# Optimization experiments

Measured on AMD Instinct MI355X. Metric: run time of the kernel, lower is better.

## Reference

```python
import jax, jax.numpy as jnp
import numpy as np

B, C, H, W = 8, 10, 128, 128  # batch, hidden_dim, spatial
EPS = 1e-5


def conv1x1(x, w, b=None):
    # x: [b, i, h, w], w: [o, i] -> [b, o, h, w]
    y = jnp.einsum('oi,bihw->bohw', w, x)
    if b is not None:
        y = y + b[None, :, None, None]
    return y


def bn(x, gamma, beta):
    # training-mode batchnorm over (N, H, W), as InPlaceABNSync(activation='none')
    m = x.mean(axis=(0, 2, 3), keepdims=True)
    v = x.var(axis=(0, 2, 3), keepdims=True)
    xn = (x - m) * jax.lax.rsqrt(v + EPS)
    return xn * gamma[None, :, None, None] + beta[None, :, None, None]


def conv_gru(x, h, wg, bg, wc):
    # ConvGRU with 1x1 kernels: gates conv -> 2 channels (reset, update)
    gates = conv1x1(jnp.concatenate([x, h], axis=1), wg, bg)  # [b,2,h,w]
    reset = jax.nn.sigmoid(gates[:, 0:1])
    update = jax.nn.sigmoid(gates[:, 1:2])
    cand = jnp.tanh(conv1x1(jnp.concatenate([x, reset * h], axis=1), wc))
    return (1.0 - update) * h + update * cand


def setup_inputs() -> dict:
    key = jax.random.key(0)
    ks = jax.random.split(key, 16)
    rn = lambda k, shape, s=1.0: jax.random.normal(k, shape, dtype=jnp.float32) * s
    inp = {
        'f0': rn(ks[0], (B, C, H, W)),
        'f1': rn(ks[1], (B, C, H, W)),
        'h0': rn(ks[2], (B, C, H, W)),
        'h1': rn(ks[3], (B, C, H, W)),
        'h2': rn(ks[4], (B, C, H, W)),
        # Composition.comp_att: Conv2d(2C -> 1, bias=True) + Sigmoid
        'W_att': rn(ks[5], (1, 2 * C), 0.1),
        'b_att': jnp.zeros((1,), jnp.float32),
        # Composition.relation: Conv(2C->2C, no bias) BN ReLU Conv(2C->C, no bias) BN ReLU
        'W_r1': rn(ks[6], (2 * C, 2 * C), 0.1),
        'g_r1': jnp.ones((2 * C,), jnp.float32),
        'be_r1': jnp.zeros((2 * C,), jnp.float32),
        'W_r2': rn(ks[7], (C, 2 * C), 0.1),
        'g_r2': jnp.ones((C,), jnp.float32),
        'be_r2': jnp.zeros((C,), jnp.float32),
        # ConvGRU update[0]: gates Conv(2C->2, bias) ; candidate Conv(2C->C, no bias)
        'Wg0': rn(ks[8], (2, 2 * C), 0.1),
        'bg0': jnp.zeros((2,), jnp.float32),
        'Wc0': rn(ks[9], (C, 2 * C), 0.1),
        # ConvGRU update[1]
        'Wg1': rn(ks[10], (2, 2 * C), 0.1),
        'bg1': jnp.zeros((2,), jnp.float32),
        'Wc1': rn(ks[11], (C, 2 * C), 0.1),
    }
    return inp


def reference(f0, f1, h0, h1, h2,
              W_att, b_att, W_r1, g_r1, be_r1, W_r2, g_r2, be_r2,
              Wg0, bg0, Wc0, Wg1, bg1, Wc1):
    # node 0: update[0](h_node_list[0], f_node_list[0])
    node0 = conv_gru(h0, f0, Wg0, bg0, Wc0)
    # Composition over children h1, h2
    comp_att = jax.nn.sigmoid(conv1x1(jnp.concatenate([h1, h2], axis=1), W_att, b_att))  # [b,1,h,w]
    x = jnp.concatenate([f1, (h1 + h2) * comp_att], axis=1)  # [b,2C,h,w]
    x = jax.nn.relu(bn(conv1x1(x, W_r1), g_r1, be_r1))
    comp_full = jax.nn.relu(bn(conv1x1(x, W_r2), g_r2, be_r2))  # [b,C,h,w]
    # node 1: update[1](comp_full, f_node_list[1])
    node1 = conv_gru(comp_full, f1, Wg1, bg1, Wc1)
    return node0, node1, comp_att
```

## Files before the change

### kernel.cpp

```cpp
#include <hip/hip_runtime.h>
#include <math.h>

#define HW     16384
#define CDIM   10
#define NPIX   131072
#define NPLANE 1310720
#define BN_N   131072.0f
#define EPS_BN 1e-5f

__device__ __forceinline__ float sigf(float x) { return 1.0f / (1.0f + __expf(-x)); }
__device__ __forceinline__ float tanh_fast(float x) {
    x = fminf(fmaxf(x, -15.0f), 15.0f);
    float e = __expf(2.0f * x);
    return (e - 1.0f) / (e + 1.0f);
}

template<int CTRL>
__device__ __forceinline__ float dpp_add(float x) {
    int t = __builtin_amdgcn_update_dpp(0, __float_as_int(x), CTRL, 0xF, 0xF, true);
    return x + __int_as_float(t);
}
__device__ __forceinline__ float wred63(float x) {
    x = dpp_add<0x111>(x);
    x = dpp_add<0x112>(x);
    x = dpp_add<0x114>(x);
    x = dpp_add<0x118>(x);
    x = dpp_add<0x142>(x);
    x = dpp_add<0x143>(x);
    return x;
}

__global__ __launch_bounds__(256) void kernA(
    const float* __restrict__ f0, const float* __restrict__ f1,
    const float* __restrict__ h0, const float* __restrict__ h1, const float* __restrict__ h2,
    const float* __restrict__ W_att, const float* __restrict__ b_att,
    const float* __restrict__ W_r1,
    const float* __restrict__ Wg0, const float* __restrict__ bg0, const float* __restrict__ Wc0,
    float* __restrict__ node0, float* __restrict__ att_out, float* __restrict__ stats1)
{
    __shared__ float sPart[4 * 40];
    const int tid = threadIdx.x;
    const int p = blockIdx.x * 256 + tid;
    const int b = p >> 14, s = p & 16383;
    const int base = b * (CDIM * HW) + s;
    const int wave = tid >> 6, lane = tid & 63;

    float vh1[10], vh2[10], vf1[10], vf0[10], vh0[10];
#pragma unroll
    for (int c = 0; c < 10; c++) {
        vh1[c] = h1[base + c * HW];
        vh2[c] = h2[base + c * HW];
        vf1[c] = f1[base + c * HW];
        vf0[c] = f0[base + c * HW];
        vh0[c] = h0[base + c * HW];
    }

    float g0 = bg0[0], g1 = bg0[1];
#pragma unroll
    for (int i = 0; i < 10; i++) {
        g0 = fmaf(Wg0[i],      vh0[i], fmaf(Wg0[10 + i], vf0[i], g0));
        g1 = fmaf(Wg0[20 + i], vh0[i], fmaf(Wg0[30 + i], vf0[i], g1));
    }
    const float r = sigf(g0), u = sigf(g1);
#pragma unroll
    for (int o = 0; o < 10; o++) {
        float acc = 0.0f;
#pragma unroll
        for (int i = 0; i < 10; i++) acc = fmaf(Wc0[o * 20 + i], vh0[i], acc);
#pragma unroll
        for (int i = 0; i < 10; i++) acc = fmaf(Wc0[o * 20 + 10 + i], r * vf0[i], acc);
        node0[base + o * HW] = (1.0f - u) * vf0[o] + u * tanh_fast(acc);
    }

    float z = b_att[0];
#pragma unroll
    for (int c = 0; c < 10; c++) z = fmaf(W_att[c], vh1[c], fmaf(W_att[10 + c], vh2[c], z));
    const float att = sigf(z);
    att_out[p] = att;

    float x[20];
#pragma unroll
    for (int c = 0; c < 10; c++) { x[c] = vf1[c]; x[10 + c] = (vh1[c] + vh2[c]) * att; }
#pragma unroll
    for (int o = 0; o < 20; o++) {
        float acc = 0.0f;
#pragma unroll
        for (int i = 0; i < 20; i++) acc = fmaf(W_r1[o * 20 + i], x[i], acc);
        float rs = wred63(acc);
        float rq = wred63(acc * acc);
        if (lane == 63) { sPart[wave * 40 + o] = rs; sPart[wave * 40 + 20 + o] = rq; }
    }
    __syncthreads();
    if (tid < 40) {
        float t = sPart[tid] + sPart[40 + tid] + sPart[80 + tid] + sPart[120 + tid];
        atomicAdd(&stats1[tid], t);
    }
}

__global__ __launch_bounds__(256) void kernC(
    const float* __restrict__ f1, const float* __restrict__ h1, const float* __restrict__ h2,
    const float* __restrict__ W_att, const float* __restrict__ b_att,
    const float* __restrict__ W_r1, const float* __restrict__ g_r1, const float* __restrict__ be_r1,
    const float* __restrict__ W_r2,
    const float* __restrict__ stats1, float* __restrict__ y2out, float* __restrict__ stats2)
{
    __shared__ float sPart[4 * 20];
    const int tid = threadIdx.x;
    const int p = blockIdx.x * 256 + tid;
    const int b = p >> 14, s = p & 16383;
    const int base = b * (CDIM * HW) + s;
    const int wave = tid >> 6, lane = tid & 63;

    float A1[20], B1[20];
#pragma unroll
    for (int c = 0; c < 20; c++) {
        float mean = stats1[c] * (1.0f / BN_N);
        float var  = stats1[20 + c] * (1.0f / BN_N) - mean * mean;
        float a = g_r1[c] * rsqrtf(var + EPS_BN);
        A1[c] = a;
        B1[c] = be_r1[c] - mean * a;
    }

    float vh1[10], vh2[10], vf1[10];
#pragma unroll
    for (int c = 0; c < 10; c++) {
        vh1[c] = h1[base + c * HW];
        vh2[c] = h2[base + c * HW];
        vf1[c] = f1[base + c * HW];
    }
    float z = b_att[0];
#pragma unroll
    for (int c = 0; c < 10; c++) z = fmaf(W_att[c], vh1[c], fmaf(W_att[10 + c], vh2[c], z));
    const float att = sigf(z);

    float x[20];
#pragma unroll
    for (int c = 0; c < 10; c++) { x[c] = vf1[c]; x[10 + c] = (vh1[c] + vh2[c]) * att; }
    float x2[20];
#pragma unroll
    for (int o = 0; o < 20; o++) {
        float acc = 0.0f;
#pragma unroll
        for (int i = 0; i < 20; i++) acc = fmaf(W_r1[o * 20 + i], x[i], acc);
        x2[o] = fmaxf(fmaf(A1[o], acc, B1[o]), 0.0f);
    }
    const int base2 = b * (10 * HW) + s;
#pragma unroll
    for (int o = 0; o < 10; o++) {
        float acc = 0.0f;
#pragma unroll
        for (int i = 0; i < 20; i++) acc = fmaf(W_r2[o * 20 + i], x2[i], acc);
        y2out[base2 + o * HW] = acc;
        float rs = wred63(acc);
        float rq = wred63(acc * acc);
        if (lane == 63) { sPart[wave * 20 + o] = rs; sPart[wave * 20 + 10 + o] = rq; }
    }
    __syncthreads();
    if (tid < 20) {
        float t = sPart[tid] + sPart[20 + tid] + sPart[40 + tid] + sPart[60 + tid];
        atomicAdd(&stats2[tid], t);
    }
}

__global__ __launch_bounds__(256) void kernE(
    const float* __restrict__ f1, const float* __restrict__ y2in,
    const float* __restrict__ stats2,
    const float* __restrict__ g_r2, const float* __restrict__ be_r2,
    const float* __restrict__ Wg1, const float* __restrict__ bg1, const float* __restrict__ Wc1,
    float* __restrict__ node1)
{
    const int tid = threadIdx.x;
    const int p = blockIdx.x * 256 + tid;
    const int b = p >> 14, s = p & 16383;
    const int base = b * (CDIM * HW) + s;

    float A2[10], B2[10];
#pragma unroll
    for (int c = 0; c < 10; c++) {
        float mean = stats2[c] * (1.0f / BN_N);
        float var  = stats2[10 + c] * (1.0f / BN_N) - mean * mean;
        float a = g_r2[c] * rsqrtf(var + EPS_BN);
        A2[c] = a;
        B2[c] = be_r2[c] - mean * a;
    }

    float comp[10], vf1[10];
#pragma unroll
    for (int c = 0; c < 10; c++) {
        vf1[c]  = f1[base + c * HW];
        comp[c] = fmaxf(fmaf(A2[c], y2in[base + c * HW], B2[c]), 0.0f);
    }
    float g0 = bg1[0], g1v = bg1[1];
#pragma unroll
    for (int i = 0; i < 10; i++) {
        g0  = fmaf(Wg1[i],      comp[i], fmaf(Wg1[10 + i], vf1[i], g0));
        g1v = fmaf(Wg1[20 + i], comp[i], fmaf(Wg1[30 + i], vf1[i], g1v));
    }
    const float r = sigf(g0), u = sigf(g1v);
#pragma unroll
    for (int o = 0; o < 10; o++) {
        float acc = 0.0f;
#pragma unroll
        for (int i = 0; i < 10; i++) acc = fmaf(Wc1[o * 20 + i], comp[i], acc);
#pragma unroll
        for (int i = 0; i < 10; i++) acc = fmaf(Wc1[o * 20 + 10 + i], r * vf1[i], acc);
        node1[base + o * HW] = (1.0f - u) * vf1[o] + u * tanh_fast(acc);
    }
}

extern "C" void kernel_launch(void* const* d_in, const int* in_sizes, int n_in,
                              void* d_out, int out_size, void* d_ws, size_t ws_size,
                              hipStream_t stream) {
    const float* f0    = (const float*)d_in[0];
    const float* f1    = (const float*)d_in[1];
    const float* h0    = (const float*)d_in[2];
    const float* h1    = (const float*)d_in[3];
    const float* h2    = (const float*)d_in[4];
    const float* W_att = (const float*)d_in[5];
    const float* b_att = (const float*)d_in[6];
    const float* W_r1  = (const float*)d_in[7];
    const float* g_r1  = (const float*)d_in[8];
    const float* be_r1 = (const float*)d_in[9];
    const float* W_r2  = (const float*)d_in[10];
    const float* g_r2  = (const float*)d_in[11];
    const float* be_r2 = (const float*)d_in[12];
    const float* Wg0   = (const float*)d_in[13];
    const float* bg0   = (const float*)d_in[14];
    const float* Wc0   = (const float*)d_in[15];
    const float* Wg1   = (const float*)d_in[16];
    const float* bg1   = (const float*)d_in[17];
    const float* Wc1   = (const float*)d_in[18];

    float* out   = (float*)d_out;
    float* node0 = out;
    float* node1 = out + NPLANE;
    float* attO  = out + 2 * NPLANE;

    float* y2     = (float*)d_ws;
    float* stats1 = y2 + (size_t)10 * NPIX;
    float* stats2 = stats1 + 40;

    hipMemsetAsync(stats1, 0, 64 * sizeof(float), stream);

    dim3 grid(NPIX / 256), blk(256);
    kernA<<<grid, blk, 0, stream>>>(f0, f1, h0, h1, h2, W_att, b_att, W_r1,
                                    Wg0, bg0, Wc0, node0, attO, stats1);
    kernC<<<grid, blk, 0, stream>>>(f1, h1, h2, W_att, b_att, W_r1, g_r1, be_r1, W_r2,
                                    stats1, y2, stats2);
    kernE<<<grid, blk, 0, stream>>>(f1, y2, stats2, g_r2, be_r2, Wg1, bg1, Wc1,
                                    node1);
}
```

Measured before the change: 148.8 us.

## Fuse three kernels into one cooperative kernel with grid-wide syncs for BN stats

Replaces the three-kernel pipeline with a single cooperative kernel of 256 blocks by 512 threads, where each thread owns one pixel. Per-block partial BN sums are written to a workspace and reduced after grid.sync(), which removes the atomics and the memset. Each thread keeps its conv activations in registers, so the recompute of attention and conv1 in the second pass, the y2 round-trip through global memory, and the reloads of f1/h1/h2 all go away. The cost is two grid-wide barriers, high register pressure from holding many live values under launch bounds of 512 threads with 2 blocks per CU, and a hard requirement that all 256 blocks be co-resident.

```diff
diff --git a/kernel.cpp b/kernel.cpp
--- a/kernel.cpp
+++ b/kernel.cpp
@@ -1,5 +1,8 @@
 #include <hip/hip_runtime.h>
+#include <hip/hip_cooperative_groups.h>
 #include <math.h>
+
+namespace cg = cooperative_groups;
 
 #define HW     16384
 #define CDIM   10
@@ -7,6 +10,8 @@
 #define NPLANE 1310720
 #define BN_N   131072.0f
 #define EPS_BN 1e-5f
+#define NBLK   256
+#define NTHR   512
 
 __device__ __forceinline__ float sigf(float x) { return 1.0f / (1.0f + __expf(-x)); }
 __device__ __forceinline__ float tanh_fast(float x) {
@@ -30,17 +35,23 @@
     return x;
 }
 
-__global__ __launch_bounds__(256) void kernA(
+__global__ __launch_bounds__(NTHR, 2) void fused(
     const float* __restrict__ f0, const float* __restrict__ f1,
     const float* __restrict__ h0, const float* __restrict__ h1, const float* __restrict__ h2,
     const float* __restrict__ W_att, const float* __restrict__ b_att,
-    const float* __restrict__ W_r1,
+    const float* __restrict__ W_r1, const float* __restrict__ g_r1, const float* __restrict__ be_r1,
+    const float* __restrict__ W_r2, const float* __restrict__ g_r2, const float* __restrict__ be_r2,
     const float* __restrict__ Wg0, const float* __restrict__ bg0, const float* __restrict__ Wc0,
-    float* __restrict__ node0, float* __restrict__ att_out, float* __restrict__ stats1)
+    const float* __restrict__ Wg1, const float* __restrict__ bg1, const float* __restrict__ Wc1,
+    float* __restrict__ node0, float* __restrict__ node1, float* __restrict__ att_out,
+    float* __restrict__ part1, float* __restrict__ part2)
 {
-    __shared__ float sPart[4 * 40];
+    cg::grid_group grid = cg::this_grid();
+    __shared__ float sPart[8 * 40];
+    __shared__ float sRed[40];
     const int tid = threadIdx.x;
-    const int p = blockIdx.x * 256 + tid;
+    const int bid = blockIdx.x;
+    const int p = bid * NTHR + tid;
     const int b = p >> 14, s = p & 16383;
     const int base = b * (CDIM * HW) + s;
     const int wave = tid >> 6, lane = tid & 63;
@@ -55,21 +66,23 @@
         vh0[c] = h0[base + c * HW];
     }
 
-    float g0 = bg0[0], g1 = bg0[1];
-#pragma unroll
-    for (int i = 0; i < 10; i++) {
-        g0 = fmaf(Wg0[i],      vh0[i], fmaf(Wg0[10 + i], vf0[i], g0));
-        g1 = fmaf(Wg0[20 + i], vh0[i], fmaf(Wg0[30 + i], vf0[i], g1));
-    }
-    const float r = sigf(g0), u = sigf(g1);
-#pragma unroll
-    for (int o = 0; o < 10; o++) {
-        float acc = 0.0f;
-#pragma unroll
-        for (int i = 0; i < 10; i++) acc = fmaf(Wc0[o * 20 + i], vh0[i], acc);
-#pragma unroll
-        for (int i = 0; i < 10; i++) acc = fmaf(Wc0[o * 20 + 10 + i], r * vf0[i], acc);
-        node0[base + o * HW] = (1.0f - u) * vf0[o] + u * tanh_fast(acc);
+    {
+        float g0 = bg0[0], g1 = bg0[1];
+#pragma unroll
+        for (int i = 0; i < 10; i++) {
+            g0 = fmaf(Wg0[i],      vh0[i], fmaf(Wg0[10 + i], vf0[i], g0));
+            g1 = fmaf(Wg0[20 + i], vh0[i], fmaf(Wg0[30 + i], vf0[i], g1));
+        }
+        const float r = sigf(g0), u = sigf(g1);
+#pragma unroll
+        for (int o = 0; o < 10; o++) {
+            float acc = 0.0f;
+#pragma unroll
+            for (int i = 0; i < 10; i++) acc = fmaf(Wc0[o * 20 + i], vh0[i], acc);
+#pragma unroll
+            for (int i = 0; i < 10; i++) acc = fmaf(Wc0[o * 20 + 10 + i], r * vf0[i], acc);
+            node0[base + o * HW] = (1.0f - u) * vf0[o] + u * tanh_fast(acc);
+        }
     }
 
     float z = b_att[0];
@@ -81,114 +94,80 @@
     float x[20];
 #pragma unroll
     for (int c = 0; c < 10; c++) { x[c] = vf1[c]; x[10 + c] = (vh1[c] + vh2[c]) * att; }
+    float acc1[20];
 #pragma unroll
     for (int o = 0; o < 20; o++) {
         float acc = 0.0f;
 #pragma unroll
         for (int i = 0; i < 20; i++) acc = fmaf(W_r1[o * 20 + i], x[i], acc);
+        acc1[o] = acc;
         float rs = wred63(acc);
         float rq = wred63(acc * acc);
         if (lane == 63) { sPart[wave * 40 + o] = rs; sPart[wave * 40 + 20 + o] = rq; }
     }
     __syncthreads();
     if (tid < 40) {
-        float t = sPart[tid] + sPart[40 + tid] + sPart[80 + tid] + sPart[120 + tid];
-        atomicAdd(&stats1[tid], t);
-    }
-}
-
-__global__ __launch_bounds__(256) void kernC(
-    const float* __restrict__ f1, const float* __restrict__ h1, const float* __restrict__ h2,
-    const float* __restrict__ W_att, const float* __restrict__ b_att,
-    const float* __restrict__ W_r1, const float* __restrict__ g_r1, const float* __restrict__ be_r1,
-    const float* __restrict__ W_r2,
-    const float* __restrict__ stats1, float* __restrict__ y2out, float* __restrict__ stats2)
-{
-    __shared__ float sPart[4 * 20];
-    const int tid = threadIdx.x;
-    const int p = blockIdx.x * 256 + tid;
-    const int b = p >> 14, s = p & 16383;
-    const int base = b * (CDIM * HW) + s;
-    const int wave = tid >> 6, lane = tid & 63;
-
+        float t = 0.0f;
+#pragma unroll
+        for (int w = 0; w < 8; w++) t += sPart[w * 40 + tid];
+        part1[tid * NBLK + bid] = t;
+    }
+    grid.sync();
+
+    for (int ch = wave; ch < 40; ch += 8) {
+        float v = part1[ch * NBLK + lane]       + part1[ch * NBLK + lane + 64]
+                + part1[ch * NBLK + lane + 128] + part1[ch * NBLK + lane + 192];
+        v = wred63(v);
+        if (lane == 63) sRed[ch] = v;
+    }
+    __syncthreads();
     float A1[20], B1[20];
 #pragma unroll
     for (int c = 0; c < 20; c++) {
-        float mean = stats1[c] * (1.0f / BN_N);
-        float var  = stats1[20 + c] * (1.0f / BN_N) - mean * mean;
+        float mean = sRed[c] * (1.0f / BN_N);
+        float var  = sRed[20 + c] * (1.0f / BN_N) - mean * mean;
         float a = g_r1[c] * rsqrtf(var + EPS_BN);
         A1[c] = a;
         B1[c] = be_r1[c] - mean * a;
     }
-
-    float vh1[10], vh2[10], vf1[10];
-#pragma unroll
-    for (int c = 0; c < 10; c++) {
-        vh1[c] = h1[base + c * HW];
-        vh2[c] = h2[base + c * HW];
-        vf1[c] = f1[base + c * HW];
-    }
-    float z = b_att[0];
-#pragma unroll
-    for (int c = 0; c < 10; c++) z = fmaf(W_att[c], vh1[c], fmaf(W_att[10 + c], vh2[c], z));
-    const float att = sigf(z);
-
-    float x[20];
-#pragma unroll
-    for (int c = 0; c < 10; c++) { x[c] = vf1[c]; x[10 + c] = (vh1[c] + vh2[c]) * att; }
     float x2[20];
 #pragma unroll
-    for (int o = 0; o < 20; o++) {
-        float acc = 0.0f;
-#pragma unroll
-        for (int i = 0; i < 20; i++) acc = fmaf(W_r1[o * 20 + i], x[i], acc);
-        x2[o] = fmaxf(fmaf(A1[o], acc, B1[o]), 0.0f);
-    }
-    const int base2 = b * (10 * HW) + s;
+    for (int o = 0; o < 20; o++) x2[o] = fmaxf(fmaf(A1[o], acc1[o], B1[o]), 0.0f);
+
+    float acc2[10];
 #pragma unroll
     for (int o = 0; o < 10; o++) {
         float acc = 0.0f;
 #pragma unroll
         for (int i = 0; i < 20; i++) acc = fmaf(W_r2[o * 20 + i], x2[i], acc);
-        y2out[base2 + o * HW] = acc;
+        acc2[o] = acc;
         float rs = wred63(acc);
         float rq = wred63(acc * acc);
         if (lane == 63) { sPart[wave * 20 + o] = rs; sPart[wave * 20 + 10 + o] = rq; }
     }
     __syncthreads();
     if (tid < 20) {
-        float t = sPart[tid] + sPart[20 + tid] + sPart[40 + tid] + sPart[60 + tid];
-        atomicAdd(&stats2[tid], t);
-    }
-}
-
-__global__ __launch_bounds__(256) void kernE(
-    const float* __restrict__ f1, const float* __restrict__ y2in,
-    const float* __restrict__ stats2,
-    const float* __restrict__ g_r2, const float* __restrict__ be_r2,
-    const float* __restrict__ Wg1, const float* __restrict__ bg1, const float* __restrict__ Wc1,
-    float* __restrict__ node1)
-{
-    const int tid = threadIdx.x;
-    const int p = blockIdx.x * 256 + tid;
-    const int b = p >> 14, s = p & 16383;
-    const int base = b * (CDIM * HW) + s;
-
-    float A2[10], B2[10];
+        float t = 0.0f;
+#pragma unroll
+        for (int w = 0; w < 8; w++) t += sPart[w * 20 + tid];
+        part2[tid * NBLK + bid] = t;
+    }
+    grid.sync();
+
+    for (int ch = wave; ch < 20; ch += 8) {
+        float v = part2[ch * NBLK + lane]       + part2[ch * NBLK + lane + 64]
+                + part2[ch * NBLK + lane + 128] + part2[ch * NBLK + lane + 192];
+        v = wred63(v);
+        if (lane == 63) sRed[ch] = v;
+    }
+    __syncthreads();
+    float comp[10];
 #pragma unroll
     for (int c = 0; c < 10; c++) {
-        float mean = stats2[c] * (1.0f / BN_N);
-        float var  = stats2[10 + c] * (1.0f / BN_N) - mean * mean;
+        float mean = sRed[c] * (1.0f / BN_N);
+        float var  = sRed[10 + c] * (1.0f / BN_N) - mean * mean;
         float a = g_r2[c] * rsqrtf(var + EPS_BN);
-        A2[c] = a;
-        B2[c] = be_r2[c] - mean * a;
-    }
-
-    float comp[10], vf1[10];
-#pragma unroll
-    for (int c = 0; c < 10; c++) {
-        vf1[c]  = f1[base + c * HW];
-        comp[c] = fmaxf(fmaf(A2[c], y2in[base + c * HW], B2[c]), 0.0f);
+        comp[c] = fmaxf(fmaf(a, acc2[c], be_r2[c] - mean * a), 0.0f);
     }
     float g0 = bg1[0], g1v = bg1[1];
 #pragma unroll
@@ -236,17 +215,19 @@
     float* node1 = out + NPLANE;
     float* attO  = out + 2 * NPLANE;
 
-    float* y2     = (float*)d_ws;
-    float* stats1 = y2 + (size_t)10 * NPIX;
-    float* stats2 = stats1 + 40;
-
-    hipMemsetAsync(stats1, 0, 64 * sizeof(float), stream);
-
-    dim3 grid(NPIX / 256), blk(256);
-    kernA<<<grid, blk, 0, stream>>>(f0, f1, h0, h1, h2, W_att, b_att, W_r1,
-                                    Wg0, bg0, Wc0, node0, attO, stats1);
-    kernC<<<grid, blk, 0, stream>>>(f1, h1, h2, W_att, b_att, W_r1, g_r1, be_r1, W_r2,
-                                    stats1, y2, stats2);
-    kernE<<<grid, blk, 0, stream>>>(f1, y2, stats2, g_r2, be_r2, Wg1, bg1, Wc1,
-                                    node1);
-}
+    float* part1 = (float*)d_ws;
+    float* part2 = part1 + 40 * NBLK;
+
+    void* args[] = {
+        (void*)&f0, (void*)&f1, (void*)&h0, (void*)&h1, (void*)&h2,
+        (void*)&W_att, (void*)&b_att,
+        (void*)&W_r1, (void*)&g_r1, (void*)&be_r1,
+        (void*)&W_r2, (void*)&g_r2, (void*)&be_r2,
+        (void*)&Wg0, (void*)&bg0, (void*)&Wc0,
+        (void*)&Wg1, (void*)&bg1, (void*)&Wc1,
+        (void*)&node0, (void*)&node1, (void*)&attO,
+        (void*)&part1, (void*)&part2
+    };
+    hipLaunchCooperativeKernel((const void*)fused, dim3(NBLK), dim3(NTHR),
+                               args, 0, stream);
+}
```

After: 210.5 us. +41.4%, slower.
